# Kernel optimization log

Hardware: AMD Instinct MI355X
Metric: run time of the kernel (lower is better)

## Reference

```python
import jax, jax.numpy as jnp
import numpy as np


def setup_inputs() -> dict:
    key = jax.random.key(0)
    k1, k2 = jax.random.split(key)
    B, T, D = 32, 512, 512
    x = jax.random.normal(k1, (B, T, D), dtype=jnp.float32)
    duration = jax.random.randint(k2, (B, T), 0, 8, dtype=jnp.int32)
    return {"x": x, "duration": duration, "max_len": 2048}


def reference(x, duration, max_len):
    """Vectorized length regulator.

    x:        [B, T, D] float
    duration: [B, T] int frames per phoneme
    max_len:  static python int, padded output length

    Returns (output [B, max_len, D], mel_lengths [B]).
    Frame t of sample b copies phoneme j where j is the first index with
    cumsum(duration)[b, j] > t (i.e. searchsorted right). Frames beyond the
    total duration are zero-padded; sequences longer than max_len are truncated
    (mel_lengths reports the untruncated length, matching the torch module,
    with the all-zero-duration edge case yielding length 1).
    """
    B, T, D = x.shape
    csum = jnp.cumsum(duration, axis=1)            # [B, T]
    dur_sum = csum[:, -1]                          # [B]
    t = jnp.arange(max_len, dtype=csum.dtype)      # [max_len]
    # phoneme index for each output frame: searchsorted(csum[b], t, 'right')
    idx = jax.vmap(lambda c: jnp.searchsorted(c, t, side='right'))(csum)  # [B, max_len]
    idx = jnp.clip(idx, 0, T - 1)
    out = jnp.take_along_axis(x, idx[:, :, None], axis=1)  # [B, max_len, D]
    valid = t[None, :] < dur_sum[:, None]                  # [B, max_len]
    out = jnp.where(valid[:, :, None], out, jnp.zeros((), dtype=x.dtype))
    mel_lengths = jnp.maximum(dur_sum, 1).astype(jnp.int32)
    return out, mel_lengths
```

## Files before the change

kernel.cpp:

```cpp
#include <hip/hip_runtime.h>


#define BB      32
#define TT      512
#define DD      512
#define MAXLEN  2048
#define CHUNK   64
#define NCHUNK  (MAXLEN / CHUNK)

typedef float f4 __attribute__((ext_vector_type(4)));

__global__ __launch_bounds__(512) void lr_fused_kernel(
    const int* __restrict__ dur, const f4* __restrict__ x,
    f4* __restrict__ out, float* __restrict__ mel_out) {
  __shared__ int s[TT];
  __shared__ int s_idx[CHUNK];

  const int b     = blockIdx.x >> 5;
  const int chunk = blockIdx.x & (NCHUNK - 1);
  const int tid   = threadIdx.x;

  s[tid] = dur[b * TT + tid];
  __syncthreads();
#pragma unroll
  for (int off = 1; off < TT; off <<= 1) {
    int v = (tid >= off) ? s[tid - off] : 0;
    __syncthreads();
    s[tid] += v;
    __syncthreads();
  }
  const int dsum = s[TT - 1];
  if (chunk == 0 && tid == 0) {
    mel_out[b] = (float)(dsum > 1 ? dsum : 1);
  }

  const int base = chunk * CHUNK;
  if (tid < CHUNK) {
    int t = base + tid;
    int v = -1;
    if (t < dsum) {
      int lo = 0, hi = TT;
      while (lo < hi) {
        int mid = (lo + hi) >> 1;
        if (s[mid] <= t) lo = mid + 1; else hi = mid;
      }
      v = lo < (TT - 1) ? lo : (TT - 1);
    }
    s_idx[tid] = v;
  }
  __syncthreads();

  const int lane = tid & 127;
  const int fsub = tid >> 7;
  const f4 zero = {0.f, 0.f, 0.f, 0.f};
#pragma unroll
  for (int it = 0; it < 16; ++it) {
    const int f = it * 4 + fsub;
    const int idx = s_idx[f];
    f4 v = zero;
    if (idx >= 0) {
      v = x[((size_t)b * TT + idx) * (DD / 4) + lane];
    }
    __builtin_nontemporal_store(
        v, &out[((size_t)b * MAXLEN + base + f) * (DD / 4) + lane]);
  }
}

extern "C" void kernel_launch(void* const* d_in, const int* in_sizes, int n_in,
                              void* d_out, int out_size, void* d_ws, size_t ws_size,
                              hipStream_t stream) {
  const float* x   = (const float*)d_in[0];
  const int*   dur = (const int*)d_in[1];
  float* out = (float*)d_out;
  float* mel_out = out + (size_t)BB * MAXLEN * DD;

  lr_fused_kernel<<<BB * NCHUNK, 512, 0, stream>>>(
      dur, (const f4*)x, (f4*)out, mel_out);
}
```

Measured before the change: 174.0 us.

## Split into scan-scatter index kernel and grid-stride gather-copy kernel

Replaces the fused kernel, in which every chunk block recomputed the 512-element prefix sum and binary searches, with two kernels. The first does one wave-shuffle scan per batch and scatters phoneme indices into a workspace frame-index table. The second is a persistent grid-stride copy that reads four indices as a vector and writes each row with nontemporal stores. This removes the redundant per-chunk scans and barriers, at the cost of a second launch and a round trip through the workspace.

```diff
diff --git a/kernel.cpp b/kernel.cpp
--- a/kernel.cpp
+++ b/kernel.cpp
@@ -5,64 +5,76 @@
 #define TT      512
 #define DD      512
 #define MAXLEN  2048
-#define CHUNK   64
-#define NCHUNK  (MAXLEN / CHUNK)
 
 typedef float f4 __attribute__((ext_vector_type(4)));
+typedef int   i4 __attribute__((ext_vector_type(4)));
 
-__global__ __launch_bounds__(512) void lr_fused_kernel(
-    const int* __restrict__ dur, const f4* __restrict__ x,
-    f4* __restrict__ out, float* __restrict__ mel_out) {
-  __shared__ int s[TT];
-  __shared__ int s_idx[CHUNK];
+__global__ __launch_bounds__(512) void lr_scan_kernel(
+    const int* __restrict__ dur, int* __restrict__ idxt,
+    float* __restrict__ mel_out) {
+  __shared__ int wsum[8];
+  const int b    = blockIdx.x;
+  const int tid  = threadIdx.x;
+  const int lane = tid & 63;
+  const int wid  = tid >> 6;
 
-  const int b     = blockIdx.x >> 5;
-  const int chunk = blockIdx.x & (NCHUNK - 1);
-  const int tid   = threadIdx.x;
-
-  s[tid] = dur[b * TT + tid];
-  __syncthreads();
+  const int d = dur[b * TT + tid];
+  int v = d;
 #pragma unroll
-  for (int off = 1; off < TT; off <<= 1) {
-    int v = (tid >= off) ? s[tid - off] : 0;
-    __syncthreads();
-    s[tid] += v;
-    __syncthreads();
+  for (int off = 1; off < 64; off <<= 1) {
+    int n = __shfl_up(v, off, 64);
+    if (lane >= off) v += n;
   }
-  const int dsum = s[TT - 1];
-  if (chunk == 0 && tid == 0) {
-    mel_out[b] = (float)(dsum > 1 ? dsum : 1);
-  }
-
-  const int base = chunk * CHUNK;
-  if (tid < CHUNK) {
-    int t = base + tid;
-    int v = -1;
-    if (t < dsum) {
-      int lo = 0, hi = TT;
-      while (lo < hi) {
-        int mid = (lo + hi) >> 1;
-        if (s[mid] <= t) lo = mid + 1; else hi = mid;
-      }
-      v = lo < (TT - 1) ? lo : (TT - 1);
-    }
-    s_idx[tid] = v;
-  }
+  if (lane == 63) wsum[wid] = v;
   __syncthreads();
 
-  const int lane = tid & 127;
-  const int fsub = tid >> 7;
+  int woff = 0, dsum = 0;
+#pragma unroll
+  for (int i = 0; i < 8; ++i) {
+    int w = wsum[i];
+    dsum += w;
+    if (i < wid) woff += w;
+  }
+  v += woff;
+
+  if (tid == 0) mel_out[b] = (float)(dsum > 1 ? dsum : 1);
+
+  int start = v - d;
+  int end   = v;
+  if (start > MAXLEN) start = MAXLEN;
+  if (end   > MAXLEN) end   = MAXLEN;
+  int* row = idxt + b * MAXLEN;
+  for (int t = start; t < end; ++t) row[t] = tid;
+  for (int t = dsum + tid; t < MAXLEN; t += TT) row[t] = -1;
+}
+
+__global__ __launch_bounds__(256) void lr_copy_kernel(
+    const int* __restrict__ idxt, const f4* __restrict__ x,
+    f4* __restrict__ out) {
+  const int lane    = threadIdx.x & 63;
+  const int gwave   = blockIdx.x * (256 / 64) + (threadIdx.x >> 6);
+  const int nwaves  = gridDim.x * (256 / 64);
+  const int ngroups = (BB * MAXLEN) / 4;
   const f4 zero = {0.f, 0.f, 0.f, 0.f};
+
+  for (int grp = gwave; grp < ngroups; grp += nwaves) {
+    const int b  = grp >> 9;
+    const int t0 = (grp & 511) * 4;
+    const i4 idx4 = *(const i4*)&idxt[b * MAXLEN + t0];
+    const f4* xb = x + (size_t)b * (TT * (DD / 4));
+    f4* ob = out + ((size_t)b * MAXLEN + t0) * (DD / 4) + lane;
 #pragma unroll
-  for (int it = 0; it < 16; ++it) {
-    const int f = it * 4 + fsub;
-    const int idx = s_idx[f];
-    f4 v = zero;
-    if (idx >= 0) {
-      v = x[((size_t)b * TT + idx) * (DD / 4) + lane];
+    for (int f = 0; f < 4; ++f) {
+      const int idx = idx4[f];
+      f4 v0 = zero, v1 = zero;
+      if (idx >= 0) {
+        const f4* xr = xb + (size_t)idx * (DD / 4) + lane;
+        v0 = xr[0];
+        v1 = xr[64];
+      }
+      __builtin_nontemporal_store(v0, ob + f * (DD / 4));
+      __builtin_nontemporal_store(v1, ob + f * (DD / 4) + 64);
     }
-    __builtin_nontemporal_store(
-        v, &out[((size_t)b * MAXLEN + base + f) * (DD / 4) + lane]);
   }
 }
 
@@ -73,7 +85,8 @@
   const int*   dur = (const int*)d_in[1];
   float* out = (float*)d_out;
   float* mel_out = out + (size_t)BB * MAXLEN * DD;
+  int* idxt = (int*)d_ws;
 
-  lr_fused_kernel<<<BB * NCHUNK, 512, 0, stream>>>(
-      dur, (const f4*)x, (f4*)out, mel_out);
+  lr_scan_kernel<<<BB, 512, 0, stream>>>(dur, idxt, mel_out);
+  lr_copy_kernel<<<2048, 256, 0, stream>>>(idxt, (const f4*)x, (f4*)out);
 }
```

Result: no change. 173.5 us (-0.3%).
